# Performance work log

Measured on AMD Instinct MI355X. Metric: run time of the kernel, lower is better.

The kernel has to match this reference:

```python
import jax, jax.numpy as jnp
import numpy as np

HIDDEN = 2048
N_HEADS = 16
N_KV_HEADS = 4
HEAD_DIM = HIDDEN // N_HEADS  # 128
N_GROUPS = N_HEADS // N_KV_HEADS  # 4


def rotate_half(x):
    # interleaved rotate: (-x_odd, x_even) interleaved back
    x_even = x[..., ::2]
    x_odd = x[..., 1::2]
    return jnp.stack((-x_odd, x_even), axis=-1).reshape(x.shape)


def setup_inputs() -> dict:
    key = jax.random.key(0)
    ks = jax.random.split(key, 8)
    B, S = 4, 2048
    x = jax.random.normal(ks[0], (B, S, HIDDEN), dtype=jnp.float32)
    # RoPE tables (precomputed cos/sin over max positions)
    inv_freq = 1.0 / (1000000.0 ** (np.arange(0, HEAD_DIM, 2, dtype=np.float32) / HEAD_DIM))
    t = np.arange(S, dtype=np.float32)
    freqs = np.outer(t, inv_freq)  # [S, HEAD_DIM/2]
    emb = np.repeat(freqs, 2, axis=-1)  # interleaved layout [S, HEAD_DIM]
    cos = jnp.asarray(np.cos(emb))
    sin = jnp.asarray(np.sin(emb))
    scale = 0.02
    Wq = jax.random.normal(ks[1], (HIDDEN, N_HEADS * HEAD_DIM), dtype=jnp.float32) * scale
    Wk = jax.random.normal(ks[2], (HIDDEN, N_KV_HEADS * HEAD_DIM), dtype=jnp.float32) * scale
    Wv = jax.random.normal(ks[3], (HIDDEN, N_KV_HEADS * HEAD_DIM), dtype=jnp.float32) * scale
    Wo = jax.random.normal(ks[4], (N_HEADS * HEAD_DIM, HIDDEN), dtype=jnp.float32) * scale
    return {"x": x, "cos": cos, "sin": sin, "Wq": Wq, "Wk": Wk, "Wv": Wv, "Wo": Wo}


def reference(x, cos, sin, Wq, Wk, Wv, Wo):
    B, S, D = x.shape
    q = (x @ Wq).reshape(B, S, N_HEADS, HEAD_DIM).transpose(0, 2, 1, 3)      # [B,H,S,d]
    k = (x @ Wk).reshape(B, S, N_KV_HEADS, HEAD_DIM).transpose(0, 2, 1, 3)   # [B,Hkv,S,d]
    v = (x @ Wv).reshape(B, S, N_KV_HEADS, HEAD_DIM).transpose(0, 2, 1, 3)
    # RoPE: position_ids = arange(S); cos/sin [S,d] -> [1,1,S,d]
    c = cos[:S][None, None, :, :]
    s = sin[:S][None, None, :, :]
    q = q * c + rotate_half(q) * s
    k = k * c + rotate_half(k) * s
    # repeat_kv: [B,Hkv,S,d] -> [B,H,S,d]
    k = jnp.repeat(k, N_GROUPS, axis=1)
    v = jnp.repeat(v, N_GROUPS, axis=1)
    # causal SDPA
    scores = jnp.einsum("bhqd,bhkd->bhqk", q, k) / jnp.sqrt(jnp.float32(HEAD_DIM))
    neg = jnp.finfo(scores.dtype).min
    causal = jnp.triu(jnp.full((S, S), neg, dtype=scores.dtype), k=1)
    scores = scores + causal[None, None]
    attn = jax.nn.softmax(scores.astype(jnp.float32), axis=-1).astype(q.dtype)
    out = jnp.einsum("bhqk,bhkd->bhqd", attn, v)
    out = out.transpose(0, 2, 1, 3).reshape(B, S, N_HEADS * HEAD_DIM)
    return out @ Wo
```

## Files before the change

kernel.cpp:

```cpp
#include <hip/hip_runtime.h>
#include <stdint.h>

#define S_LEN 2048
#define BATCH 4
#define HID   2048
#define HD    128
#define NKV   4
#define MTOT  (BATCH*S_LEN)
#define NQT2  (S_LEN/256)
#define QSCALE 0.08838834764831845f
#define LOG2E  1.4426950408889634f

#define EXP2F(x) __builtin_amdgcn_exp2f(x)

typedef float    f32x4  __attribute__((ext_vector_type(4)));
typedef __bf16   bf16x8 __attribute__((ext_vector_type(8)));
typedef __bf16   bf16x4 __attribute__((ext_vector_type(4)));
typedef unsigned u32x2  __attribute__((ext_vector_type(2)));

__device__ __forceinline__ void gld16(const void* g, void* l) {
    __builtin_amdgcn_global_load_lds(
        (const __attribute__((address_space(1))) void*)g,
        (__attribute__((address_space(3))) void*)l, 16, 0, 0);
}

__global__ void k_conv_x(const float* __restrict__ in, __bf16* __restrict__ out) {
    int i = blockIdx.x * blockDim.x + threadIdx.x;
    f32x4 a = ((const f32x4*)in)[2 * i];
    f32x4 b = ((const f32x4*)in)[2 * i + 1];
    bf16x8 o;
    o[0] = (__bf16)a[0]; o[1] = (__bf16)a[1]; o[2] = (__bf16)a[2]; o[3] = (__bf16)a[3];
    o[4] = (__bf16)b[0]; o[5] = (__bf16)b[1]; o[6] = (__bf16)b[2]; o[7] = (__bf16)b[3];
    ((bf16x8*)out)[i] = o;
}

__global__ void k_transpose_all(const float* __restrict__ Wq,
                                const float* __restrict__ Wk,
                                const float* __restrict__ Wv,
                                const float* __restrict__ Wo,
                                __bf16* __restrict__ wqt,
                                __bf16* __restrict__ wkvt,
                                __bf16* __restrict__ wot) {
    const int z = blockIdx.z;
    const float* in; __bf16* out; int N;
    if      (z == 0) { in = Wq; out = wqt;  N = 2048; }
    else if (z == 1) { in = Wk; out = wkvt; N = 512;  }
    else if (z == 2) { in = Wv; out = wkvt + (size_t)512 * HID; N = 512; }
    else             { in = Wo; out = wot;  N = 2048; }
    int k0 = blockIdx.x * 64, n0 = blockIdx.y * 64;
    if (n0 >= N) return;
    __shared__ float tile[64][65];
    for (int e = threadIdx.x; e < 4096; e += 256) {
        int r = e >> 6, c = e & 63;
        tile[r][c] = in[(size_t)(k0 + r) * N + n0 + c];
    }
    __syncthreads();
    for (int e = threadIdx.x; e < 4096; e += 256) {
        int r = e >> 6, c = e & 63;
        out[(size_t)(n0 + r) * HID + k0 + c] = (__bf16)tile[c][r];
    }
}

#define BARM asm volatile("s_barrier" ::: "memory")
#define BAR1 do { BARM;                                                       \
                  asm volatile("s_waitcnt lgkmcnt(0)" ::: "memory");          \
                  __builtin_amdgcn_sched_barrier(0); } while (0)
#define BAR2 BARM
#define MM(qm, qn)                                                            \
    do {                                                                      \
        __builtin_amdgcn_s_setprio(1);                                        \
        _Pragma("unroll") for (int ks = 0; ks < 2; ks++)                      \
        _Pragma("unroll") for (int mf = 0; mf < 4; mf++)                      \
        _Pragma("unroll") for (int nf = 0; nf < 2; nf++)                      \
            acc[qm][qn][mf][nf] = __builtin_amdgcn_mfma_f32_16x16x32_bf16(    \
                af[mf][ks], bf[nf][ks], acc[qm][qn][mf][nf], 0, 0, 0);        \
        __builtin_amdgcn_s_setprio(0);                                        \
    } while (0)

#define GEMM8_BODY(Aptr, Bptr)                                                \
    __shared__ __bf16 Ab[2][2][128 * 64];                                     \
    __shared__ __bf16 Bb[2][2][128 * 64];                                     \
    const int tid = threadIdx.x, lane = tid & 63, wave = tid >> 6;            \
    const int wm = wave >> 2, wn = wave & 3;                                  \
    const int lo = lane & 15, hi = lane >> 4;                                 \
    f32x4 acc[2][2][4][2] = {};                                               \
    const int srow = wave * 8 + (lane >> 3);                                  \
    const int sp   = lane & 7;                                                \
    auto STA = [&](int s, int h, int t) {                                     \
        _Pragma("unroll") for (int p = 0; p < 2; p++) {                       \
            int rr = p * 64 + srow;                                           \
            int c = sp ^ (rr & 7);                                            \
            gld16(Aptr + (size_t)(m0 + h * 128 + rr) * HID + t * 64 + c * 8,  \
                  &Ab[s][h][(p * 64 + wave * 8) * 64]);                       \
        }                                                                     \
    };                                                                        \
    auto STB = [&](int s, int h, int t) {                                     \
        _Pragma("unroll") for (int p = 0; p < 2; p++) {                       \
            int rr = p * 64 + srow;                                           \
            int c = sp ^ (rr & 7);                                            \
            gld16(Bptr + (size_t)(n0 + h * 128 + rr) * HID + t * 64 + c * 8,  \
                  &Bb[s][h][(p * 64 + wave * 8) * 64]);                       \
        }                                                                     \
    };                                                                        \
    bf16x8 af[4][2], bf[2][2];                                                \
    auto LDA = [&](int s, int qm) {                                           \
        _Pragma("unroll") for (int mf = 0; mf < 4; mf++) {                    \
            int rr = wm * 64 + mf * 16 + lo;                                  \
            _Pragma("unroll") for (int ks = 0; ks < 2; ks++) {                \
                int pp = (ks * 4 + hi) ^ (rr & 7);                            \
                af[mf][ks] = *(const bf16x8*)&Ab[s][qm][rr * 64 + pp * 8];    \
            }                                                                 \
        }                                                                     \
    };                                                                        \
    auto LDB = [&](int s, int qn) {                                           \
        _Pragma("unroll") for (int nf = 0; nf < 2; nf++) {                    \
            int rr = wn * 32 + nf * 16 + lo;                                  \
            _Pragma("unroll") for (int ks = 0; ks < 2; ks++) {                \
                int pp = (ks * 4 + hi) ^ (rr & 7);                            \
                bf[nf][ks] = *(const bf16x8*)&Bb[s][qn][rr * 64 + pp * 8];    \
            }                                                                 \
        }                                                                     \
    };                                                                        \
    STA(0, 0, 0); STB(0, 0, 0); STA(0, 1, 0); STB(0, 1, 0);                   \
    STA(1, 1, 1); STB(1, 1, 1);                                               \
    asm volatile("s_waitcnt vmcnt(4)" ::: "memory");                          \
    BARM;                                                                     \
    _Pragma("unroll 1")                                                       \
    for (int i = 0; i < 16; i++) {                                            \
        const int t0 = 2 * i, t1 = 2 * i + 1;                                 \
        const bool more = (i < 15);                                           \
        LDA(0, 0); LDB(0, 0);                                                 \
        STA(1, 0, t1); STB(1, 0, t1);                                         \
        BAR1; MM(0, 0); BAR2;                                                 \
        LDB(0, 1);                                                            \
        BAR1; MM(0, 1); BAR2;                                                 \
        LDA(0, 1); LDB(0, 0);                                                 \
        if (more) STA(0, 0, t0 + 2);                                          \
        BAR1; MM(1, 0); BAR2;                                                 \
        LDB(0, 1);                                                            \
        if (more) STB(0, 0, t0 + 2);                                          \
        BAR1; MM(1, 1);                                                       \
        if (more) { asm volatile("s_waitcnt vmcnt(4)" ::: "memory"); }        \
        else      { asm volatile("s_waitcnt vmcnt(0)" ::: "memory"); }        \
        BAR2;                                                                 \
        LDA(1, 1); LDB(1, 1);                                                 \
        if (more) { STA(0, 1, t0 + 2); STB(0, 1, t0 + 2); }                   \
        BAR1; MM(1, 1); BAR2;                                                 \
        LDB(1, 0);                                                            \
        BAR1; MM(1, 0); BAR2;                                                 \
        LDA(1, 0); LDB(1, 1);                                                 \
        if (more) STA(1, 1, t1 + 2);                                          \
        BAR1; MM(0, 1); BAR2;                                                 \
        LDB(1, 0);                                                            \
        if (more) STB(1, 1, t1 + 2);                                          \
        BAR1; MM(0, 0);                                                       \
        if (more) { asm volatile("s_waitcnt vmcnt(4)" ::: "memory"); }        \
        BAR2;                                                                 \
    }

__global__ __launch_bounds__(512) void k_gemm_q8(const __bf16* __restrict__ A,
                                                 const __bf16* __restrict__ Bt,
                                                 unsigned char* __restrict__ qb8,
                                                 const float* __restrict__ cosp,
                                                 const float* __restrict__ sinp) {
    const int m0 = (blockIdx.x >> 3) * 256;
    const int n0 = (blockIdx.x & 7) * 256;
    GEMM8_BODY(A, Bt)

    __bf16* Cs = (__bf16*)&Ab[0][0][0];
    const int crow = tid >> 4;
    const int cch  = tid & 15;
    const int d0 = cch * 8;
    const float QS2 = QSCALE * LOG2E;
#pragma unroll
    for (int qm = 0; qm < 2; qm++)
#pragma unroll
        for (int qn = 0; qn < 2; qn++) {
#pragma unroll
            for (int mf = 0; mf < 4; mf++)
#pragma unroll
                for (int nf = 0; nf < 2; nf++) {
                    int rl = wm * 64 + mf * 16 + hi * 4;
                    int cl = wn * 32 + nf * 16 + lo;
#pragma unroll
                    for (int r = 0; r < 4; r++)
                        Cs[(rl + r) * 132 + cl] = (__bf16)acc[qm][qn][mf][nf][r];
                }
            __syncthreads();
#pragma unroll
            for (int rep = 0; rep < 4; rep++) {
                int row = rep * 32 + crow;
                int rowg = m0 + qm * 128 + row;
                int colg = n0 + qn * 128 + cch * 8;
                bf16x8 v = *(const bf16x8*)&Cs[row * 132 + cch * 8];
                float f[8];
#pragma unroll
                for (int j = 0; j < 8; j++) f[j] = (float)v[j];
                int s = rowg & (S_LEN - 1);
                f32x4 c0 = *(const f32x4*)&cosp[s * HD + d0];
                f32x4 c1 = *(const f32x4*)&cosp[s * HD + d0 + 4];
                f32x4 s0 = *(const f32x4*)&sinp[s * HD + d0];
                f32x4 s1 = *(const f32x4*)&sinp[s * HD + d0 + 4];
                float cc[8] = {c0[0], c0[1], c0[2], c0[3], c1[0], c1[1], c1[2], c1[3]};
                float ss[8] = {s0[0], s0[1], s0[2], s0[3], s1[0], s1[1], s1[2], s1[3]};
#pragma unroll
                for (int p = 0; p < 4; p++) {
                    float e0 = f[2 * p], e1 = f[2 * p + 1];
                    f[2 * p]     = (e0 * cc[2 * p]     - e1 * ss[2 * p])     * QS2;
                    f[2 * p + 1] = (e1 * cc[2 * p + 1] + e0 * ss[2 * p + 1]) * QS2;
                }
                int u0 = __builtin_amdgcn_cvt_pk_fp8_f32(f[0], f[1], 0, false);
                u0     = __builtin_amdgcn_cvt_pk_fp8_f32(f[2], f[3], u0, true);
                int u1 = __builtin_amdgcn_cvt_pk_fp8_f32(f[4], f[5], 0, false);
                u1     = __builtin_amdgcn_cvt_pk_fp8_f32(f[6], f[7], u1, true);
                u32x2 pk; pk[0] = (unsigned)u0; pk[1] = (unsigned)u1;
                *(u32x2*)&qb8[(size_t)rowg * HID + colg] = pk;
            }
            __syncthreads();
        }
}

__global__ __launch_bounds__(512) void k_gemm_o8(const __bf16* __restrict__ A,
                                                 const __bf16* __restrict__ Bt,
                                                 float* __restrict__ Cp) {
    const int m0 = (blockIdx.x >> 3) * 256;
    const int n0 = (blockIdx.x & 7) * 256;
    GEMM8_BODY(A, Bt)

#pragma unroll
    for (int qm = 0; qm < 2; qm++)
#pragma unroll
        for (int qn = 0; qn < 2; qn++)
#pragma unroll
            for (int mf = 0; mf < 4; mf++)
#pragma unroll
                for (int nf = 0; nf < 2; nf++) {
                    int row = m0 + qm * 128 + wm * 64 + mf * 16 + hi * 4;
                    int col = n0 + qn * 128 + wn * 32 + nf * 16 + lo;
#pragma unroll
                    for (int r = 0; r < 4; r++)
                        Cp[(size_t)(row + r) * HID + col] = acc[qm][qn][mf][nf][r];
                }
}

__global__ __launch_bounds__(256) void k_gemm_kv(const __bf16* __restrict__ A,
                                                 const __bf16* __restrict__ Bt,
                                                 unsigned char* __restrict__ kb8,
                                                 __bf16* __restrict__ vtb,
                                                 const float* __restrict__ cosp,
                                                 const float* __restrict__ sinp) {
    __shared__ __align__(16) char smem[33792];
    __bf16* As = (__bf16*)smem;
    __bf16* Bs = (__bf16*)(smem + 16384);
    const int tid = threadIdx.x, lane = tid & 63, wave = tid >> 6;
    const int wm = wave >> 1, wn = wave & 1;
    const int m0 = blockIdx.x * 128;
    const int n0 = 2048 + blockIdx.y * 128;
    const int lo = lane & 15, hi = lane >> 4;
    f32x4 acc[4][4] = {};

    const int srow = wave * 8 + (lane >> 3);
    const int sp   = lane & 7;

    for (int kt = 0; kt < HID; kt += 64) {
#pragma unroll
        for (int r = 0; r < 4; r++) {
            int row = r * 32 + srow;
            int c = sp ^ (row & 7);
            gld16(A + (size_t)(m0 + row) * HID + kt + c * 8, &As[(r * 32 + wave * 8) * 64]);
        }
#pragma unroll
        for (int r = 0; r < 4; r++) {
            int row = r * 32 + srow;
            int c = sp ^ (row & 7);
            gld16(Bt + (size_t)(n0 + row) * HID + kt + c * 8, &Bs[(r * 32 + wave * 8) * 64]);
        }
        __syncthreads();
#pragma unroll
        for (int ks = 0; ks < 2; ks++) {
            bf16x8 af[4], bfr[4];
#pragma unroll
            for (int mt = 0; mt < 4; mt++) {
                int row = wm * 64 + mt * 16 + lo;
                int pp = (ks * 4 + hi) ^ (row & 7);
                af[mt] = *(const bf16x8*)&As[row * 64 + pp * 8];
            }
#pragma unroll
            for (int nt = 0; nt < 4; nt++) {
                int row = wn * 64 + nt * 16 + lo;
                int pp = (ks * 4 + hi) ^ (row & 7);
                bfr[nt] = *(const bf16x8*)&Bs[row * 64 + pp * 8];
            }
#pragma unroll
            for (int mt = 0; mt < 4; mt++)
#pragma unroll
                for (int nt = 0; nt < 4; nt++)
                    acc[mt][nt] = __builtin_amdgcn_mfma_f32_16x16x32_bf16(
                        af[mt], bfr[nt], acc[mt][nt], 0, 0, 0);
        }
        __syncthreads();
    }

    if (n0 < 2560) {
        __bf16* Cs = (__bf16*)smem;
#pragma unroll
        for (int mt = 0; mt < 4; mt++)
#pragma unroll
            for (int nt = 0; nt < 4; nt++) {
                int rl = wm * 64 + mt * 16 + hi * 4;
                int cl = wn * 64 + nt * 16 + lo;
#pragma unroll
                for (int r = 0; r < 4; r++)
                    Cs[(rl + r) * 132 + cl] = (__bf16)acc[mt][nt][r];
            }
        __syncthreads();

        const int crow = tid >> 4;
        const int cch  = tid & 15;
        const int colg = n0 + cch * 8;
        const int d0 = colg & (HD - 1);
#pragma unroll
        for (int rep = 0; rep < 8; rep++) {
            int row = rep * 16 + crow;
            int rowg = m0 + row;
            bf16x8 v = *(const bf16x8*)&Cs[row * 132 + cch * 8];
            float f[8];
#pragma unroll
            for (int j = 0; j < 8; j++) f[j] = (float)v[j];
            int s = rowg & (S_LEN - 1);
            f32x4 c0 = *(const f32x4*)&cosp[s * HD + d0];
            f32x4 c1 = *(const f32x4*)&cosp[s * HD + d0 + 4];
            f32x4 s0 = *(const f32x4*)&sinp[s * HD + d0];
            f32x4 s1 = *(const f32x4*)&sinp[s * HD + d0 + 4];
            float cc[8] = {c0[0], c0[1], c0[2], c0[3], c1[0], c1[1], c1[2], c1[3]};
            float ss[8] = {s0[0], s0[1], s0[2], s0[3], s1[0], s1[1], s1[2], s1[3]};
#pragma unroll
            for (int p = 0; p < 4; p++) {
                float e0 = f[2 * p], e1 = f[2 * p + 1];
                f[2 * p]     = e0 * cc[2 * p]     - e1 * ss[2 * p];
                f[2 * p + 1] = e1 * cc[2 * p + 1] + e0 * ss[2 * p + 1];
            }
            int u0 = __builtin_amdgcn_cvt_pk_fp8_f32(f[0], f[1], 0, false);
            u0     = __builtin_amdgcn_cvt_pk_fp8_f32(f[2], f[3], u0, true);
            int u1 = __builtin_amdgcn_cvt_pk_fp8_f32(f[4], f[5], 0, false);
            u1     = __builtin_amdgcn_cvt_pk_fp8_f32(f[6], f[7], u1, true);
            u32x2 pk; pk[0] = (unsigned)u0; pk[1] = (unsigned)u1;
            *(u32x2*)&kb8[(size_t)rowg * 512 + (colg - 2048)] = pk;
        }
    } else {
        __bf16* CsT = (__bf16*)smem;
#pragma unroll
        for (int mt = 0; mt < 4; mt++)
#pragma unroll
            for (int nt = 0; nt < 4; nt++) {
                int cl = wn * 64 + nt * 16 + lo;
                int mrow = wm * 64 + mt * 16 + hi * 4;
                bf16x4 w;
#pragma unroll
                for (int r = 0; r < 4; r++) w[r] = (__bf16)acc[mt][nt][r];
                *(bf16x4*)&CsT[cl * 132 + mrow] = w;
            }
        __syncthreads();

        const int kvh = (n0 - 2560) >> 7;
        const int bb = m0 >> 11;
        const int s0 = m0 & (S_LEN - 1);
        __bf16* dst = vtb + (size_t)(bb * NKV + kvh) * HD * S_LEN;
        const int dloc = tid >> 4;
        const int sch  = tid & 15;
#pragma unroll
        for (int rep = 0; rep < 8; rep++) {
            int d = rep * 16 + dloc;
            bf16x8 v = *(const bf16x8*)&CsT[d * 132 + sch * 8];
            *(bf16x8*)&dst[(size_t)d * S_LEN + s0 + sch * 8] = v;
        }
    }
}

__global__ __launch_bounds__(512) void k_attn(const unsigned char* __restrict__ qb8,
                                              const unsigned char* __restrict__ kb8,
                                              const __bf16* __restrict__ vtb,
                                              __bf16* __restrict__ ob) {
    __shared__ char   Ks8[2][128 * 128];
    __shared__ __bf16 Vs[2][128 * 128];
    __shared__ __bf16 Ps[8][2048];
    const int tid = threadIdx.x, lane = tid & 63, wave = tid >> 6;
    const int pair = blockIdx.x, h = blockIdx.y, b = blockIdx.z;
    const int kvh = h >> 2;
    const int lo = lane & 15, hi = lane >> 4;
    char* PsW = (char*)&Ps[wave][0];

    const unsigned char* kbb = kb8 + (size_t)b * S_LEN * 512 + kvh * HD;
    const __bf16* vbb = vtb + (size_t)(b * NKV + kvh) * HD * S_LEN;

    const int krow_s = tid >> 3;
    const int kp_s   = tid & 7;
    const int vrow_s = tid >> 4;
    const int vp_s   = tid & 15;

    auto STAGE_K = [&](int buf, int t) {
#pragma unroll
        for (int r = 0; r < 2; r++) {
            int row = r * 64 + krow_s;
            int c = kp_s ^ (row & 7);
            gld16(kbb + (size_t)(t * 128 + row) * 512 + c * 16,
                  &Ks8[buf][(r * 64 + wave * 8) * 128]);
        }
    };
    auto STAGE_V = [&](int buf, int t) {
#pragma unroll
        for (int r = 0; r < 4; r++) {
            int row = r * 32 + vrow_s;
            int c = vp_s ^ (row & 15);
            gld16(vbb + (size_t)row * S_LEN + t * 128 + c * 8,
                  &Vs[buf][(r * 32 + wave * 4) * 128]);
        }
    };

    auto SM = [&](f32x4 (&sc)[8], float& Mr, float& Lr, f32x4 (&o)[8]) {
        float mloc = sc[0][0];
#pragma unroll
        for (int nt = 0; nt < 8; nt++)
#pragma unroll
            for (int r = 0; r < 4; r++) mloc = fmaxf(mloc, sc[nt][r]);
        mloc = fmaxf(mloc, __shfl_xor(mloc, 16, 64));
        mloc = fmaxf(mloc, __shfl_xor(mloc, 32, 64));
        float mn = (mloc <= Mr + 8.f) ? Mr : mloc;
        float sum = 0.f;
#pragma unroll
        for (int nt = 0; nt < 8; nt++)
#pragma unroll
            for (int r = 0; r < 4; r++) {
                float e = EXP2F(sc[nt][r] - mn);
                sc[nt][r] = e;
                sum += e;
            }
        sum += __shfl_xor(sum, 16, 64);
        sum += __shfl_xor(sum, 32, 64);
        if (mn != Mr) {
            float scl = EXP2F(Mr - mn);
            Lr = Lr * scl + sum;
            Mr = mn;
#pragma unroll
            for (int dt = 0; dt < 8; dt++) o[dt] *= scl;
        } else {
            Lr += sum;
        }
    };

#pragma unroll 1
    for (int pi = 0; pi < 2; pi++) {
        const int qt = pi ? (NQT2 - 1 - pair) : pair;
        const int nkv = 2 * qt + 2;
        const int qbase = qt * 256 + wave * 32;

        const unsigned char* qp0 = qb8 + (size_t)(b * S_LEN + qbase + lo) * HID + h * HD;
        const unsigned char* qp1 = qp0 + (size_t)16 * HID;
        long qa0[4], qa1[4];
#pragma unroll
        for (int kf = 0; kf < 4; kf++) {
            qa0[kf] = *(const long*)(qp0 + kf * 32 + hi * 8);
            qa1[kf] = *(const long*)(qp1 + kf * 32 + hi * 8);
        }

        f32x4 o0[8] = {}, o1[8] = {};
        float Mr0 = -3e30f, Lr0 = 0.f, Mr1 = -3e30f, Lr1 = 0.f;

        int cur = 0;
        if (pi == 1) __syncthreads();
        STAGE_K(0, 0);
        STAGE_V(0, 0);
        __syncthreads();

#pragma unroll 1
        for (int t = 0; t < nkv; t++) {
            if (t < nkv - 1) { STAGE_K(cur ^ 1, t + 1); STAGE_V(cur ^ 1, t + 1); }

            f32x4 sc0[8], sc1[8];
            __builtin_amdgcn_s_setprio(1);
#pragma unroll
            for (int nt = 0; nt < 8; nt++) {
                f32x4 a = {0.f, 0.f, 0.f, 0.f}, bb = {0.f, 0.f, 0.f, 0.f};
#pragma unroll
                for (int kf = 0; kf < 4; kf++) {
                    int row = nt * 16 + lo;
                    int lch = 2 * kf + (hi >> 1);
                    long kf8 = *(const long*)&Ks8[cur][row * 128 +
                                ((lch ^ (row & 7)) * 16) + (hi & 1) * 8];
                    a  = __builtin_amdgcn_mfma_f32_16x16x32_fp8_fp8(kf8, qa0[kf], a, 0, 0, 0);
                    bb = __builtin_amdgcn_mfma_f32_16x16x32_fp8_fp8(kf8, qa1[kf], bb, 0, 0, 0);
                }
                sc0[nt] = a; sc1[nt] = bb;
            }
            __builtin_amdgcn_s_setprio(0);

            if (t * 128 + 127 > qbase) {
                int qg = qbase + lo;
#pragma unroll
                for (int nt = 0; nt < 8; nt++)
#pragma unroll
                    for (int r = 0; r < 4; r++) {
                        int kg = t * 128 + nt * 16 + hi * 4 + r;
                        if (kg > qg) sc0[nt][r] = -1e30f;
                    }
            }
            if (t * 128 + 127 > qbase + 16) {
                int qg = qbase + 16 + lo;
#pragma unroll
                for (int nt = 0; nt < 8; nt++)
#pragma unroll
                    for (int r = 0; r < 4; r++) {
                        int kg = t * 128 + nt * 16 + hi * 4 + r;
                        if (kg > qg) sc1[nt][r] = -1e30f;
                    }
            }

            SM(sc0, Mr0, Lr0, o0);
            SM(sc1, Mr1, Lr1, o1);

#pragma unroll
            for (int hh = 0; hh < 2; hh++) {
#pragma unroll
                for (int ntl = 0; ntl < 4; ntl++) {
                    int nt = hh * 4 + ntl;
                    bf16x4 p0, p1;
#pragma unroll
                    for (int r = 0; r < 4; r++) { p0[r] = (__bf16)sc0[nt][r]; p1[r] = (__bf16)sc1[nt][r]; }
                    int off = lo * 128 + ((ntl * 32 + hi * 8) ^ ((lo & 7) << 4));
                    *(bf16x4*)(PsW + off)        = p0;
                    *(bf16x4*)(PsW + 2048 + off) = p1;
                }
                bf16x8 pf0[2], pf1[2];
#pragma unroll
                for (int c = 0; c < 2; c++) {
                    int off = lo * 128 + ((c * 64 + hi * 16) ^ ((lo & 7) << 4));
                    pf0[c] = *(const bf16x8*)(PsW + off);
                    pf1[c] = *(const bf16x8*)(PsW + 2048 + off);
                }
                __builtin_amdgcn_s_setprio(1);
#pragma unroll
                for (int dt = 0; dt < 8; dt++) {
                    int rowd = dt * 16 + lo;
#pragma unroll
                    for (int c = 0; c < 2; c++) {
                        int gch = hh * 8 + c * 4 + hi;
                        bf16x8 vv = *(const bf16x8*)&Vs[cur][rowd * 128 +
                                     (gch ^ (rowd & 15)) * 8];
                        o0[dt] = __builtin_amdgcn_mfma_f32_16x16x32_bf16(vv, pf0[c], o0[dt], 0, 0, 0);
                        o1[dt] = __builtin_amdgcn_mfma_f32_16x16x32_bf16(vv, pf1[c], o1[dt], 0, 0, 0);
                    }
                }
                __builtin_amdgcn_s_setprio(0);
            }
            __syncthreads();
            cur ^= 1;
        }

        const int qe = lane >> 2, c4 = lane & 3;
#pragma unroll
        for (int sub = 0; sub < 2; sub++) {
            float rl = 1.0f / (sub ? Lr1 : Lr0);
            char* Pp = PsW + sub * 2048;
#pragma unroll
            for (int h2 = 0; h2 < 2; h2++) {
#pragma unroll
                for (int dt4 = 0; dt4 < 4; dt4++) {
                    f32x4 ov = sub ? o1[h2 * 4 + dt4] : o0[h2 * 4 + dt4];
                    bf16x4 w;
#pragma unroll
                    for (int r = 0; r < 4; r++) w[r] = (__bf16)(ov[r] * rl);
                    *(bf16x4*)(Pp + lo * 128 + ((dt4 * 32 + hi * 8) ^ ((lo & 7) << 4))) = w;
                }
#pragma unroll
                for (int s2 = 0; s2 < 2; s2++) {
                    int ch = c4 + s2 * 4;
                    bf16x8 v = *(const bf16x8*)(Pp + qe * 128 + ((ch * 16) ^ ((qe & 7) << 4)));
                    int qg = qbase + sub * 16 + qe;
                    int col = h * HD + h2 * 64 + ch * 8;
                    *(bf16x8*)&ob[(size_t)(b * S_LEN + qg) * HID + col] = v;
                }
            }
        }
    }
}

extern "C" void kernel_launch(void* const* d_in, const int* in_sizes, int n_in,
                              void* d_out, int out_size, void* d_ws, size_t ws_size,
                              hipStream_t stream) {
    (void)in_sizes; (void)n_in; (void)out_size; (void)ws_size;
    const float* x    = (const float*)d_in[0];
    const float* cosp = (const float*)d_in[1];
    const float* sinp = (const float*)d_in[2];
    const float* Wq   = (const float*)d_in[3];
    const float* Wk   = (const float*)d_in[4];
    const float* Wv   = (const float*)d_in[5];
    const float* Wo   = (const float*)d_in[6];
    float* out = (float*)d_out;

    char* ws = (char*)d_ws;
    __bf16*        xb   = (__bf16*)(ws);
    __bf16*        wqt  = (__bf16*)(ws + 33554432);
    __bf16*        wkvt = (__bf16*)(ws + 41943040);
    __bf16*        wot  = (__bf16*)(ws + 46137344);
    unsigned char* qb8  = (unsigned char*)(ws + 54525952);
    unsigned char* kb8  = (unsigned char*)(ws + 71303168);
    __bf16*        vtb  = (__bf16*)(ws + 75497472);
    __bf16*        aob  = xb;

    k_conv_x<<<MTOT * HID / 8 / 256, 256, 0, stream>>>(x, xb);
    { dim3 g(32, 32, 4);
      k_transpose_all<<<g, 256, 0, stream>>>(Wq, Wk, Wv, Wo, wqt, wkvt, wot); }

    k_gemm_q8<<<256, 512, 0, stream>>>(xb, wqt, qb8, cosp, sinp);
    { dim3 g(64, 8); k_gemm_kv<<<g, 256, 0, stream>>>(xb, wqt, kb8, vtb, cosp, sinp); }

    { dim3 g(NQT2 / 2, 16, BATCH); k_attn<<<g, 512, 0, stream>>>(qb8, kb8, vtb, aob); }

    k_gemm_o8<<<256, 512, 0, stream>>>(aob, wot, out);
}
```

Before: 302.9 us.

## Rewrite KV projection GEMM as 8-wave double-buffered pipelined kernel

```diff
diff --git a/kernel.cpp b/kernel.cpp
--- a/kernel.cpp
+++ b/kernel.cpp
@@ -243,125 +243,157 @@
                 }
 }
 
-__global__ __launch_bounds__(256) void k_gemm_kv(const __bf16* __restrict__ A,
-                                                 const __bf16* __restrict__ Bt,
-                                                 unsigned char* __restrict__ kb8,
-                                                 __bf16* __restrict__ vtb,
-                                                 const float* __restrict__ cosp,
-                                                 const float* __restrict__ sinp) {
-    __shared__ __align__(16) char smem[33792];
-    __bf16* As = (__bf16*)smem;
-    __bf16* Bs = (__bf16*)(smem + 16384);
+__global__ __launch_bounds__(512) void k_gemm_kv8(const __bf16* __restrict__ A,
+                                                  const __bf16* __restrict__ Bt,
+                                                  unsigned char* __restrict__ kb8,
+                                                  __bf16* __restrict__ vtb,
+                                                  const float* __restrict__ cosp,
+                                                  const float* __restrict__ sinp) {
+    __shared__ __bf16 Ab[2][2][128 * 64];
+    __shared__ __bf16 Bb[2][128 * 64];
     const int tid = threadIdx.x, lane = tid & 63, wave = tid >> 6;
-    const int wm = wave >> 1, wn = wave & 1;
-    const int m0 = blockIdx.x * 128;
-    const int n0 = 2048 + blockIdx.y * 128;
+    const int wm = wave >> 2, wn = wave & 3;
+    const int m0 = (blockIdx.x >> 3) * 256;
+    const int n0 = 2048 + (blockIdx.x & 7) * 128;
     const int lo = lane & 15, hi = lane >> 4;
-    f32x4 acc[4][4] = {};
+    f32x4 acc[2][4][2] = {};
 
     const int srow = wave * 8 + (lane >> 3);
     const int sp   = lane & 7;
 
-    for (int kt = 0; kt < HID; kt += 64) {
-#pragma unroll
-        for (int r = 0; r < 4; r++) {
-            int row = r * 32 + srow;
-            int c = sp ^ (row & 7);
-            gld16(A + (size_t)(m0 + row) * HID + kt + c * 8, &As[(r * 32 + wave * 8) * 64]);
-        }
-#pragma unroll
-        for (int r = 0; r < 4; r++) {
-            int row = r * 32 + srow;
-            int c = sp ^ (row & 7);
-            gld16(Bt + (size_t)(n0 + row) * HID + kt + c * 8, &Bs[(r * 32 + wave * 8) * 64]);
-        }
-        __syncthreads();
-#pragma unroll
-        for (int ks = 0; ks < 2; ks++) {
-            bf16x8 af[4], bfr[4];
-#pragma unroll
-            for (int mt = 0; mt < 4; mt++) {
-                int row = wm * 64 + mt * 16 + lo;
-                int pp = (ks * 4 + hi) ^ (row & 7);
-                af[mt] = *(const bf16x8*)&As[row * 64 + pp * 8];
-            }
-#pragma unroll
-            for (int nt = 0; nt < 4; nt++) {
-                int row = wn * 64 + nt * 16 + lo;
-                int pp = (ks * 4 + hi) ^ (row & 7);
-                bfr[nt] = *(const bf16x8*)&Bs[row * 64 + pp * 8];
-            }
-#pragma unroll
-            for (int mt = 0; mt < 4; mt++)
-#pragma unroll
-                for (int nt = 0; nt < 4; nt++)
-                    acc[mt][nt] = __builtin_amdgcn_mfma_f32_16x16x32_bf16(
-                        af[mt], bfr[nt], acc[mt][nt], 0, 0, 0);
-        }
-        __syncthreads();
+    auto STA = [&](int s, int h, int t) {
+#pragma unroll
+        for (int p = 0; p < 2; p++) {
+            int rr = p * 64 + srow;
+            int c = sp ^ (rr & 7);
+            gld16(A + (size_t)(m0 + h * 128 + rr) * HID + t * 64 + c * 8,
+                  &Ab[s][h][(p * 64 + wave * 8) * 64]);
+        }
+    };
+    auto STB = [&](int s, int t) {
+#pragma unroll
+        for (int p = 0; p < 2; p++) {
+            int rr = p * 64 + srow;
+            int c = sp ^ (rr & 7);
+            gld16(Bt + (size_t)(n0 + rr) * HID + t * 64 + c * 8,
+                  &Bb[s][(p * 64 + wave * 8) * 64]);
+        }
+    };
+
+    bf16x8 af[4][2], bf[2][2];
+    auto LDA = [&](int s, int qm) {
+#pragma unroll
+        for (int mf = 0; mf < 4; mf++) {
+            int rr = wm * 64 + mf * 16 + lo;
+#pragma unroll
+            for (int ks = 0; ks < 2; ks++) {
+                int pp = (ks * 4 + hi) ^ (rr & 7);
+                af[mf][ks] = *(const bf16x8*)&Ab[s][qm][rr * 64 + pp * 8];
+            }
+        }
+    };
+    auto LDB = [&](int s) {
+#pragma unroll
+        for (int nf = 0; nf < 2; nf++) {
+            int rr = wn * 32 + nf * 16 + lo;
+#pragma unroll
+            for (int ks = 0; ks < 2; ks++) {
+                int pp = (ks * 4 + hi) ^ (rr & 7);
+                bf[nf][ks] = *(const bf16x8*)&Bb[s][rr * 64 + pp * 8];
+            }
+        }
+    };
+
+#define MMKV(qm)                                                              \
+    do {                                                                      \
+        __builtin_amdgcn_s_setprio(1);                                        \
+        _Pragma("unroll") for (int ks = 0; ks < 2; ks++)                      \
+        _Pragma("unroll") for (int mf = 0; mf < 4; mf++)                      \
+        _Pragma("unroll") for (int nf = 0; nf < 2; nf++)                      \
+            acc[qm][mf][nf] = __builtin_amdgcn_mfma_f32_16x16x32_bf16(        \
+                af[mf][ks], bf[nf][ks], acc[qm][mf][nf], 0, 0, 0);            \
+        __builtin_amdgcn_s_setprio(0);                                        \
+    } while (0)
+
+    STA(0, 0, 0); STA(0, 1, 0); STB(0, 0);
+    STA(1, 0, 1);
+    asm volatile("s_waitcnt vmcnt(2)" ::: "memory");
+    BARM;
+
+#pragma unroll 1
+    for (int i = 0; i < 16; i++) {
+        const int t0 = 2 * i, t1 = 2 * i + 1;
+        const bool more = (i < 15);
+        LDA(0, 0); LDB(0);
+        STA(1, 1, t1); STB(1, t1);
+        BAR1; MMKV(0); BAR2;
+        LDA(0, 1);
+        if (more) { STA(0, 0, t0 + 2); STB(0, t0 + 2); }
+        BAR1; MMKV(1);
+        if (more) { asm volatile("s_waitcnt vmcnt(4)" ::: "memory"); }
+        else      { asm volatile("s_waitcnt vmcnt(0)" ::: "memory"); }
+        BAR2;
+        LDA(1, 0); LDB(1);
+        if (more) STA(0, 1, t0 + 2);
+        BAR1; MMKV(0); BAR2;
+        LDA(1, 1);
+        if (more) STA(1, 0, t1 + 2);
+        BAR1; MMKV(1);
+        if (more) { asm volatile("s_waitcnt vmcnt(2)" ::: "memory"); }
+        BAR2;
     }
 
     if (n0 < 2560) {
-        __bf16* Cs = (__bf16*)smem;
-#pragma unroll
-        for (int mt = 0; mt < 4; mt++)
-#pragma unroll
-            for (int nt = 0; nt < 4; nt++) {
-                int rl = wm * 64 + mt * 16 + hi * 4;
-                int cl = wn * 64 + nt * 16 + lo;
-#pragma unroll
-                for (int r = 0; r < 4; r++)
-                    Cs[(rl + r) * 132 + cl] = (__bf16)acc[mt][nt][r];
-            }
-        __syncthreads();
-
+        __bf16* Cs = (__bf16*)&Ab[0][0][0];
         const int crow = tid >> 4;
         const int cch  = tid & 15;
-        const int colg = n0 + cch * 8;
-        const int d0 = colg & (HD - 1);
-#pragma unroll
-        for (int rep = 0; rep < 8; rep++) {
-            int row = rep * 16 + crow;
-            int rowg = m0 + row;
-            bf16x8 v = *(const bf16x8*)&Cs[row * 132 + cch * 8];
-            float f[8];
-#pragma unroll
-            for (int j = 0; j < 8; j++) f[j] = (float)v[j];
-            int s = rowg & (S_LEN - 1);
-            f32x4 c0 = *(const f32x4*)&cosp[s * HD + d0];
-            f32x4 c1 = *(const f32x4*)&cosp[s * HD + d0 + 4];
-            f32x4 s0 = *(const f32x4*)&sinp[s * HD + d0];
-            f32x4 s1 = *(const f32x4*)&sinp[s * HD + d0 + 4];
-            float cc[8] = {c0[0], c0[1], c0[2], c0[3], c1[0], c1[1], c1[2], c1[3]};
-            float ss[8] = {s0[0], s0[1], s0[2], s0[3], s1[0], s1[1], s1[2], s1[3]};
-#pragma unroll
-            for (int p = 0; p < 4; p++) {
-                float e0 = f[2 * p], e1 = f[2 * p + 1];
-                f[2 * p]     = e0 * cc[2 * p]     - e1 * ss[2 * p];
-                f[2 * p + 1] = e1 * cc[2 * p + 1] + e0 * ss[2 * p + 1];
-            }
-            int u0 = __builtin_amdgcn_cvt_pk_fp8_f32(f[0], f[1], 0, false);
-            u0     = __builtin_amdgcn_cvt_pk_fp8_f32(f[2], f[3], u0, true);
-            int u1 = __builtin_amdgcn_cvt_pk_fp8_f32(f[4], f[5], 0, false);
-            u1     = __builtin_amdgcn_cvt_pk_fp8_f32(f[6], f[7], u1, true);
-            u32x2 pk; pk[0] = (unsigned)u0; pk[1] = (unsigned)u1;
-            *(u32x2*)&kb8[(size_t)rowg * 512 + (colg - 2048)] = pk;
+        const int d0 = cch * 8;
+#pragma unroll
+        for (int qm = 0; qm < 2; qm++) {
+#pragma unroll
+            for (int mf = 0; mf < 4; mf++)
+#pragma unroll
+                for (int nf = 0; nf < 2; nf++) {
+                    int rl = wm * 64 + mf * 16 + hi * 4;
+                    int cl = wn * 32 + nf * 16 + lo;
+#pragma unroll
+                    for (int r = 0; r < 4; r++)
+                        Cs[(rl + r) * 132 + cl] = (__bf16)acc[qm][mf][nf][r];
+                }
+            __syncthreads();
+#pragma unroll
+            for (int rep = 0; rep < 4; rep++) {
+                int row = rep * 32 + crow;
+                int rowg = m0 + qm * 128 + row;
+                int colg = n0 + cch * 8;
+                bf16x8 v = *(const bf16x8*)&Cs[row * 132 + cch * 8];
+                float f[8];
+#pragma unroll
+                for (int j = 0; j < 8; j++) f[j] = (float)v[j];
+                int s = rowg & (S_LEN - 1);
+                f32x4 c0 = *(const f32x4*)&cosp[s * HD + d0];
+                f32x4 c1 = *(const f32x4*)&cosp[s * HD + d0 + 4];
+                f32x4 s0 = *(const f32x4*)&sinp[s * HD + d0];
+                f32x4 s1 = *(const f32x4*)&sinp[s * HD + d0 + 4];
+                float cc[8] = {c0[0], c0[1], c0[2], c0[3], c1[0], c1[1], c1[2], c1[3]};
+                float ss[8] = {s0[0], s0[1], s0[2], s0[3], s1[0], s1[1], s1[2], s1[3]};
+#pragma unroll
+                for (int p = 0; p < 4; p++) {
+                    float e0 = f[2 * p], e1 = f[2 * p + 1];
+                    f[2 * p]     = e0 * cc[2 * p]     - e1 * ss[2 * p];
+                    f[2 * p + 1] = e1 * cc[2 * p + 1] + e0 * ss[2 * p + 1];
+                }
+                int u0 = __builtin_amdgcn_cvt_pk_fp8_f32(f[0], f[1], 0, false);
+                u0     = __builtin_amdgcn_cvt_pk_fp8_f32(f[2], f[3], u0, true);
+                int u1 = __builtin_amdgcn_cvt_pk_fp8_f32(f[4], f[5], 0, false);
+                u1     = __builtin_amdgcn_cvt_pk_fp8_f32(f[6], f[7], u1, true);
+                u32x2 pk; pk[0] = (unsigned)u0; pk[1] = (unsigned)u1;
+                *(u32x2*)&kb8[(size_t)rowg * 512 + (colg - 2048)] = pk;
+            }
+            __syncthreads();
         }
     } else {
-        __bf16* CsT = (__bf16*)smem;
-#pragma unroll
-        for (int mt = 0; mt < 4; mt++)
-#pragma unroll
-            for (int nt = 0; nt < 4; nt++) {
-                int cl = wn * 64 + nt * 16 + lo;
-                int mrow = wm * 64 + mt * 16 + hi * 4;
-                bf16x4 w;
-#pragma unroll
-                for (int r = 0; r < 4; r++) w[r] = (__bf16)acc[mt][nt][r];
-                *(bf16x4*)&CsT[cl * 132 + mrow] = w;
-            }
-        __syncthreads();
-
+        __bf16* CsT = (__bf16*)&Ab[0][0][0];
         const int kvh = (n0 - 2560) >> 7;
         const int bb = m0 >> 11;
         const int s0 = m0 & (S_LEN - 1);
@@ -369,12 +401,29 @@
         const int dloc = tid >> 4;
         const int sch  = tid & 15;
 #pragma unroll
-        for (int rep = 0; rep < 8; rep++) {
-            int d = rep * 16 + dloc;
-            bf16x8 v = *(const bf16x8*)&CsT[d * 132 + sch * 8];
-            *(bf16x8*)&dst[(size_t)d * S_LEN + s0 + sch * 8] = v;
+        for (int qm = 0; qm < 2; qm++) {
+#pragma unroll
+            for (int mf = 0; mf < 4; mf++)
+#pragma unroll
+                for (int nf = 0; nf < 2; nf++) {
+                    int cl = wn * 32 + nf * 16 + lo;
+                    int mrow = wm * 64 + mf * 16 + hi * 4;
+                    bf16x4 w;
+#pragma unroll
+                    for (int r = 0; r < 4; r++) w[r] = (__bf16)acc[qm][mf][nf][r];
+                    *(bf16x4*)&CsT[cl * 132 + mrow] = w;
+                }
+            __syncthreads();
+#pragma unroll
+            for (int rep = 0; rep < 4; rep++) {
+                int d = rep * 32 + dloc;
+                bf16x8 v = *(const bf16x8*)&CsT[d * 132 + sch * 8];
+                *(bf16x8*)&dst[(size_t)d * S_LEN + s0 + qm * 128 + sch * 8] = v;
+            }
+            __syncthreads();
         }
     }
+#undef MMKV
 }
 
 __global__ __launch_bounds__(512) void k_attn(const unsigned char* __restrict__ qb8,
@@ -612,7 +661,7 @@
       k_transpose_all<<<g, 256, 0, stream>>>(Wq, Wk, Wv, Wo, wqt, wkvt, wot); }
 
     k_gemm_q8<<<256, 512, 0, stream>>>(xb, wqt, qb8, cosp, sinp);
-    { dim3 g(64, 8); k_gemm_kv<<<g, 256, 0, stream>>>(xb, wqt, kb8, vtb, cosp, sinp); }
+    k_gemm_kv8<<<256, 512, 0, stream>>>(xb, wqt, kb8, vtb, cosp, sinp);
 
     { dim3 g(NQT2 / 2, 16, BATCH); k_attn<<<g, 512, 0, stream>>>(qb8, kb8, vtb, aob); }
 
```

Result: slower. 312.4 us (+3.1%).
